# Kernel optimization log

Hardware: AMD Instinct MI355X
Metric: run time of the kernel (lower is better)

The kernel has to match this reference:

```python
import jax, jax.numpy as jnp
import numpy as np
from math import sqrt

THRESHOLD = 0.5
NEG_POS_RATIO = 3
ALPHA = 1.0


def make_priors():
    fms = [(38, 0.1, [1.0, 2.0, 0.5]), (19, 0.2, [1.0, 2.0, 0.5, 3.0, 1.0 / 3]),
           (10, 0.375, [1.0, 2.0, 0.5, 3.0, 1.0 / 3]), (5, 0.55, [1.0, 2.0, 0.5, 3.0, 1.0 / 3]),
           (3, 0.725, [1.0, 2.0, 0.5]), (1, 0.9, [1.0, 2.0, 0.5])]
    scales = [0.1, 0.2, 0.375, 0.55, 0.725, 0.9]
    priors = []
    for k, (d, s, ratios) in enumerate(fms):
        for i in range(d):
            for j in range(d):
                cx = (i + 0.5) / d
                cy = (j + 0.5) / d
                for r in ratios:
                    priors.append([cx, cy, s * sqrt(r), s / sqrt(r)])
                    if r == 1.0:
                        add = sqrt(scales[k] * scales[k + 1]) if k + 1 < len(scales) else 1.0
                        priors.append([cx, cy, add, add])
    return np.clip(np.asarray(priors, dtype=np.float32), 0.0, 1.0)  # [8732, 4]


def cxcy_to_xy(b):
    return jnp.concatenate([b[..., :2] - b[..., 2:] / 2.0, b[..., :2] + b[..., 2:] / 2.0], -1)


def jaccard(a, b):
    # a: [O,4] cxcy, b: [P,4] cxcy -> IoU [O,P]
    a_xy, b_xy = cxcy_to_xy(a), cxcy_to_xy(b)
    lt = jnp.maximum(a_xy[:, None, :2], b_xy[None, :, :2])
    rb = jnp.minimum(a_xy[:, None, 2:], b_xy[None, :, 2:])
    wh = jnp.clip(rb - lt, 0.0)
    inter = wh[..., 0] * wh[..., 1]
    area_a = (a_xy[:, 2] - a_xy[:, 0]) * (a_xy[:, 3] - a_xy[:, 1])
    area_b = (b_xy[:, 2] - b_xy[:, 0]) * (b_xy[:, 3] - b_xy[:, 1])
    return inter / (area_a[:, None] + area_b[None, :] - inter)


def cxcy_to_gcxgcy(cxcy, priors):
    g_cxcy = (cxcy[..., :2] - priors[..., :2]) / (priors[..., 2:] / 10.0)
    g_wh = jnp.log(cxcy[..., 2:] / priors[..., 2:]) * 5.0
    return jnp.concatenate([g_cxcy, g_wh], -1)


def match_one(boxes_i, priors):
    # boxes_i: [O,4] cxcy
    n_obj = boxes_i.shape[0]
    ov = jaccard(boxes_i, priors)                      # [O, P]
    ov_per_prior = ov.max(0)                           # [P]
    obj_per_prior = ov.argmax(0)                       # [P]
    prior_per_obj = ov.argmax(1)                       # [O]
    obj_per_prior = obj_per_prior.at[prior_per_obj].set(jnp.arange(n_obj))
    ov_per_prior = ov_per_prior.at[prior_per_obj].set(1.0)
    labels = (ov_per_prior >= THRESHOLD).astype(jnp.int32)  # [P], 1=text 0=bg
    true_locs = cxcy_to_gcxgcy(boxes_i[obj_per_prior], priors)  # [P,4]
    return labels, true_locs


def setup_inputs() -> dict:
    key = jax.random.key(0)
    k1, k2, k3, k4 = jax.random.split(key, 4)
    priors = jnp.asarray(make_priors())
    B, P, O = 512, priors.shape[0], 16
    predicted_locs = jax.random.normal(k1, (B, P, 4), dtype=jnp.float32)
    predicted_scores = jax.random.normal(k2, (B, P, 2), dtype=jnp.float32)
    centers = 0.2 + 0.6 * jax.random.uniform(k3, (B, O, 2), dtype=jnp.float32)
    wh = 0.05 + 0.35 * jax.random.uniform(k4, (B, O, 2), dtype=jnp.float32)
    boxes = jnp.concatenate([centers, wh], -1)  # cxcy format
    return {"predicted_locs": predicted_locs, "predicted_scores": predicted_scores,
            "boxes": boxes, "priors": priors}


def reference(predicted_locs, predicted_scores, boxes, priors):
    B, P, _ = predicted_locs.shape
    labels, true_locs = jax.vmap(match_one, in_axes=(0, None))(boxes, priors)  # [B,P], [B,P,4]
    pos = labels != 0
    mask = pos.astype(predicted_locs.dtype)            # [B,P]
    n_pos = pos.sum(1)                                 # [B]

    # localization L1 loss (mean over positive box coordinates)
    loc_abs = jnp.abs(predicted_locs - true_locs).sum(-1)  # [B,P]
    loc_loss = (loc_abs * mask).sum() / (mask.sum() * 4.0)

    # per-prior cross-entropy
    logp = jax.nn.log_softmax(predicted_scores, -1)
    ce = -jnp.take_along_axis(logp, labels[..., None], -1)[..., 0]  # [B,P]

    conf_pos = (ce * mask).sum()
    ce_neg = jnp.where(pos, 0.0, ce)
    ce_neg = jnp.sort(ce_neg, axis=1)[:, ::-1]         # descending
    hard = jnp.arange(P)[None, :] < (NEG_POS_RATIO * n_pos)[:, None]
    conf_hn = (ce_neg * hard.astype(ce_neg.dtype)).sum()
    conf_loss = (conf_pos + conf_hn) / n_pos.sum().astype(predicted_locs.dtype)
    return conf_loss + ALPHA * loc_loss
```

## Files before the change

kernel.cpp:

```cpp
#include <hip/hip_runtime.h>

#define NP 8732
#define NQ (NP / 4)
#define NPT 35
#define NO 16
#define BLK 256
#define NWAVE (BLK / 64)
#define SPLIT 4
#define CHUNK (NP / SPLIT)
#define NITER ((CHUNK + BLK - 1) / BLK)
#define BLKS 1024
#define NWAVES (BLKS / 64)
#define NPT2 9


__device__ __forceinline__ float rfl(float x) {
    return __uint_as_float(__builtin_amdgcn_readfirstlane(__float_as_uint(x)));
}

__global__ __launch_bounds__(BLK, 4) void match_kernel(
    const float* __restrict__ boxes,
    const float* __restrict__ priors,
    unsigned char* __restrict__ g_obj,
    float* __restrict__ g_bv,
    int*   __restrict__ g_bi)
{
    const int b    = blockIdx.x;
    const int s    = blockIdx.y;
    const int tid  = threadIdx.x;
    const int lane = tid & 63;
    const int wv   = tid >> 6;
    const int lo = s * CHUNK, hi = lo + CHUNK;

    __shared__ float s_pv[NWAVE][NO][16];
    __shared__ int   s_pi[NWAVE][NO][16];

    float sx0[NO], sy0[NO], sx1[NO], sy1[NO], ra[NO];
    {
        const float4* bx4 = (const float4*)(boxes + (size_t)b * NO * 4);
#pragma unroll
        for (int j = 0; j < NO; j++) {
            float4 o = bx4[j];
            float hx = o.z * 0.5f, hy = o.w * 0.5f;
            sx0[j] = rfl(o.x - hx); sy0[j] = rfl(o.y - hy);
            sx1[j] = rfl(o.x + hx); sy1[j] = rfl(o.y + hy);
            ra[j]  = o.z * o.w;
        }
    }

    float tbv[NO]; int tbp[NO];
#pragma unroll
    for (int j = 0; j < NO; j++) { tbv[j] = -1.0f; tbp[j] = lo; }

    unsigned char* obj_row = g_obj + (size_t)b * NP;
    for (int k = 0; k < NITER; k++) {
        int p0 = lo + tid + k * BLK;
        bool valid = p0 < hi;
        int p = valid ? p0 : hi - 1;
        float4 pr = ((const float4*)priors)[p];
        float px0 = pr.x - pr.z * 0.5f, py0 = pr.y - pr.w * 0.5f;
        float px1 = pr.x + pr.z * 0.5f, py1 = pr.y + pr.w * 0.5f;
        float areab = pr.z * pr.w;
        if (!valid) px0 = 4.0f;
        float bv = -1.0f; int bo = 0;
#pragma unroll
        for (int j = 0; j < NO; j++) {
            bool ov = (sx1[j] >= px0) && (px1 >= sx0[j]) &&
                      (sy1[j] >= py0) && (py1 >= sy0[j]);
            if (ov) {
                float ix0 = fmaxf(sx0[j], px0);
                float iy0 = fmaxf(sy0[j], py0);
                float ix1 = fminf(sx1[j], px1);
                float iy1 = fminf(sy1[j], py1);
                float iw = fmaxf(ix1 - ix0, 0.0f);
                float ih = fmaxf(iy1 - iy0, 0.0f);
                float inter = iw * ih;
                float den = ra[j] + areab - inter;
                float iou = inter * __builtin_amdgcn_rcpf(den);
                if (iou > bv)     { bv = iou; bo = j; }
                if (iou > tbv[j]) { tbv[j] = iou; tbp[j] = p; }
            }
        }
        if (valid) obj_row[p] = (unsigned char)(bo | ((bv >= 0.5f) ? 0x80 : 0));
    }

#pragma unroll
    for (int j = 0; j < NO; j++) {
        float v = tbv[j]; int i = tbp[j];
        float v2 = __shfl_down(v, 32, 64); int i2 = __shfl_down(i, 32, 64);
        if (v2 > v || (v2 == v && i2 < i)) { v = v2; i = i2; }
        v2 = __shfl_down(v, 16, 64); i2 = __shfl_down(i, 16, 64);
        if (v2 > v || (v2 == v && i2 < i)) { v = v2; i = i2; }
        if (lane < 16) { s_pv[wv][j][lane] = v; s_pi[wv][j][lane] = i; }
    }
    __syncthreads();
    {
        const int j = tid >> 4, e = tid & 15;
        float v = s_pv[0][j][e]; int i = s_pi[0][j][e];
#pragma unroll
        for (int w = 1; w < NWAVE; w++) {
            float v2 = s_pv[w][j][e]; int i2 = s_pi[w][j][e];
            if (v2 > v || (v2 == v && i2 < i)) { v = v2; i = i2; }
        }
#pragma unroll
        for (int off = 8; off >= 1; off >>= 1) {
            float v2 = __shfl_down(v, off, 16); int i2 = __shfl_down(i, off, 16);
            if (v2 > v || (v2 == v && i2 < i)) { v = v2; i = i2; }
        }
        if (e == 0) {
            g_bv[((size_t)b * NO + j) * SPLIT + s] = v;
            g_bi[((size_t)b * NO + j) * SPLIT + s] = i;
        }
    }
}

__device__ __forceinline__ int hist_select(unsigned* hist, unsigned* s_part,
                                           unsigned* s_csuf, unsigned* s_sel,
                                           unsigned& kk, int tid, int lane, int wv)
{
    if (tid < 256) {
        unsigned ps = 0;
#pragma unroll
        for (int i = 0; i < 16; i++) ps += hist[tid * 16 + i];
        s_part[tid] = ps;
    }
    __syncthreads();
    if (wv == 0) {
        unsigned c0 = s_part[4 * lane + 0], c1 = s_part[4 * lane + 1];
        unsigned c2 = s_part[4 * lane + 2], c3 = s_part[4 * lane + 3];
        unsigned g = c0 + c1 + c2 + c3;
        unsigned incl = g;
#pragma unroll
        for (int off = 1; off < 64; off <<= 1) {
            unsigned o = __shfl_down(incl, off, 64);
            if (lane + off < 64) incl += o;
        }
        unsigned excl = incl - g;
        s_csuf[4 * lane + 3] = excl;
        s_csuf[4 * lane + 2] = excl + c3;
        s_csuf[4 * lane + 1] = excl + c3 + c2;
        s_csuf[4 * lane + 0] = excl + c3 + c2 + c1;
    }
    __syncthreads();
    if (tid < 256) {
        unsigned base = s_csuf[tid];
        if (base < kk && kk <= base + s_part[tid]) {
            unsigned run = base;
            for (int i = 15; i >= 0; i--) {
                unsigned h = hist[tid * 16 + i];
                if (kk <= run + h) { s_sel[0] = (unsigned)(tid * 16 + i); s_sel[1] = kk - run; break; }
                run += h;
            }
        }
    }
    __syncthreads();
    kk = s_sel[1];
    return (int)s_sel[0];
}

__global__ __launch_bounds__(BLKS, 8) void loss2_kernel(
    const float* __restrict__ plocs,
    const float* __restrict__ pscores,
    const float* __restrict__ boxes,
    const float* __restrict__ priors,
    const unsigned char* __restrict__ g_obj,
    const float* __restrict__ g_bv,
    const int*   __restrict__ g_bi,
    float* __restrict__ loc_out,
    float* __restrict__ conf_out,
    int*   __restrict__ npos_out)
{
    const int b    = blockIdx.x;
    const int tid  = threadIdx.x;
    const int lane = tid & 63;
    const int wv   = tid >> 6;

    __shared__ unsigned char s_obj[NP];
    __shared__ unsigned s_hist[4096];
    __shared__ unsigned s_part[256];
    __shared__ unsigned s_csuf[256];
    __shared__ unsigned s_sel[2];
    __shared__ float s_bcw[NO][4];
    __shared__ int   s_bestp[NO];
    __shared__ float s_tval;
    __shared__ float s_fred[3 * NWAVES];
    __shared__ int   s_ired[NWAVES];

    const unsigned* objw = (const unsigned*)(g_obj + (size_t)b * NP);
    for (int i = tid; i < NP / 4; i += BLKS) ((unsigned*)s_obj)[i] = objw[i];
    if (tid < NO * 4) ((float*)s_bcw)[tid] = boxes[(size_t)b * NO * 4 + tid];
    if (tid < NO) {
        const float* bv = g_bv + ((size_t)b * NO + tid) * SPLIT;
        const int*   bi = g_bi + ((size_t)b * NO + tid) * SPLIT;
        float v = bv[0]; int i = bi[0];
#pragma unroll
        for (int s = 1; s < SPLIT; s++) {
            float v2 = bv[s]; int i2 = bi[s];
            if (v2 > v || (v2 == v && i2 < i)) { v = v2; i = i2; }
        }
        s_bestp[tid] = i;
    }
    __syncthreads();
    if (tid == 0) {
#pragma unroll
        for (int o = 0; o < NO; o++) s_obj[s_bestp[o]] = (unsigned char)(0x80 | o);
    }
    __syncthreads();

    float ce[NPT2];
    float loc_sum = 0.0f, conf_pos = 0.0f; int np = 0;
    const float2* sc2 = (const float2*)(pscores + (size_t)b * NP * 2);
    const float4* pl4 = (const float4*)(plocs  + (size_t)b * NP * 4);
#pragma unroll
    for (int k = 0; k < NPT2; k++) {
        int p = tid + k * BLKS;
        float v = 0.0f;
        if (p < NP) {
            unsigned m = s_obj[p];
            bool pos = (m & 0x80) != 0;
            float2 s = sc2[p];
            float mx = fmaxf(s.x, s.y);
            float dd = fabsf(s.x - s.y);
            float cev = mx + __logf(1.0f + __expf(-dd)) - (pos ? s.y : s.x);
            if (pos) {
                np++;
                conf_pos += cev;
                int o = m & 15;
                float4 pr = ((const float4*)priors)[p];
                float gx = (s_bcw[o][0] - pr.x) / (pr.z / 10.0f);
                float gy = (s_bcw[o][1] - pr.y) / (pr.w / 10.0f);
                float gw = __logf(s_bcw[o][2] / pr.z) * 5.0f;
                float gh = __logf(s_bcw[o][3] / pr.w) * 5.0f;
                float4 pl = pl4[p];
                loc_sum += fabsf(pl.x - gx) + fabsf(pl.y - gy)
                         + fabsf(pl.z - gw) + fabsf(pl.w - gh);
            } else {
                v = cev;
            }
        }
        ce[k] = v;
    }

    int npw = np;
    for (int off = 32; off; off >>= 1) npw += __shfl_down(npw, off, 64);
    if (lane == 0) s_ired[wv] = npw;
    __syncthreads();
    int n_pos = 0;
#pragma unroll
    for (int w = 0; w < NWAVES; w++) n_pos += s_ired[w];

    const int K = 3 * n_pos;
    const bool selAll = (K >= NP);
    float t = 0.0f;
    if (!selAll) {
        unsigned kk = (unsigned)K;
        for (int i = tid; i < 4096; i += BLKS) s_hist[i] = 0u;
        __syncthreads();
#pragma unroll
        for (int k = 0; k < NPT2; k++)
            atomicAdd(&s_hist[__float_as_uint(ce[k]) >> 19], 1u);
        __syncthreads();
        unsigned b1 = (unsigned)hist_select(s_hist, s_part, s_csuf, s_sel, kk, tid, lane, wv);
        unsigned cnt1 = s_hist[b1];
        if (cnt1 == 1u) {
#pragma unroll
            for (int k = 0; k < NPT2; k++)
                if ((__float_as_uint(ce[k]) >> 19) == b1) s_tval = ce[k];
            __syncthreads();
            t = s_tval;
        } else {
            __syncthreads();
            for (int i = tid; i < 4096; i += BLKS) s_hist[i] = 0u;
            __syncthreads();
#pragma unroll
            for (int k = 0; k < NPT2; k++) {
                unsigned u = __float_as_uint(ce[k]);
                if ((u >> 19) == b1) atomicAdd(&s_hist[(u >> 7) & 0xFFFu], 1u);
            }
            __syncthreads();
            unsigned b2 = (unsigned)hist_select(s_hist, s_part, s_csuf, s_sel, kk, tid, lane, wv);
            unsigned p2 = (b1 << 12) | b2;
            unsigned cnt2 = s_hist[b2];
            if (cnt2 == 1u) {
#pragma unroll
                for (int k = 0; k < NPT2; k++)
                    if ((__float_as_uint(ce[k]) >> 7) == p2) s_tval = ce[k];
                __syncthreads();
                t = s_tval;
            } else {
                __syncthreads();
                for (int i = tid; i < 4096; i += BLKS) s_hist[i] = 0u;
                __syncthreads();
#pragma unroll
                for (int k = 0; k < NPT2; k++) {
                    unsigned u = __float_as_uint(ce[k]);
                    if ((u >> 7) == p2) atomicAdd(&s_hist[u & 0x7Fu], 1u);
                }
                __syncthreads();
                unsigned b3 = (unsigned)hist_select(s_hist, s_part, s_csuf, s_sel, kk, tid, lane, wv);
                t = __uint_as_float((p2 << 7) | b3);
            }
        }
    }

    float sgt = 0.0f; int cgt = 0;
#pragma unroll
    for (int k = 0; k < NPT2; k++) {
        float v = ce[k];
        if (selAll || v > t) { sgt += v; cgt++; }
    }

    float a = sgt, c = conf_pos, l = loc_sum; int g = cgt;
    for (int off = 32; off; off >>= 1) {
        a += __shfl_down(a, off, 64);
        c += __shfl_down(c, off, 64);
        l += __shfl_down(l, off, 64);
        g += __shfl_down(g, off, 64);
    }
    __syncthreads();
    if (lane == 0) {
        s_fred[wv] = a; s_fred[NWAVES + wv] = c; s_fred[2 * NWAVES + wv] = l;
        s_ired[wv] = g;
    }
    __syncthreads();
    if (tid == 0) {
        float sa = 0.0f, sc = 0.0f, sl = 0.0f; int sg = 0;
#pragma unroll
        for (int w = 0; w < NWAVES; w++) {
            sa += s_fred[w]; sc += s_fred[NWAVES + w]; sl += s_fred[2 * NWAVES + w];
            sg += s_ired[w];
        }
        float conf_hn = selAll ? sa : (sa + (float)(K - sg) * t);
        conf_out[b] = sc + conf_hn;
        loc_out[b]  = sl;
        npos_out[b] = n_pos;
    }
}

__global__ __launch_bounds__(BLK, 2) void mbox_row_kernel(
    const float* __restrict__ plocs, const float* __restrict__ pscores,
    const float* __restrict__ boxes, const float* __restrict__ priors,
    float* __restrict__ loc_out, float* __restrict__ conf_out,
    int* __restrict__ npos_out)
{
    const int b = blockIdx.x, tid = threadIdx.x, lane = tid & 63, wv = tid >> 6;
    const int par = tid & 1, objLo = par << 3;
    __shared__ __align__(16) float s_ce[NP];
    __shared__ unsigned char s_obj[NP];
    __shared__ float s_bcw[NO][4], s_bxy[NO][4], s_barea[NO];
    __shared__ float s_redv[NO * NWAVE]; __shared__ int s_redi[NO * NWAVE];
    __shared__ int s_bestp[NO];
    __shared__ unsigned s_hist16[16];
    __shared__ float s_tval;
    __shared__ float s_fred[3 * NWAVE]; __shared__ int s_ired[NWAVE];

    if (tid < NO * 4) ((float*)s_bcw)[tid] = boxes[(size_t)b * NO * 4 + tid];
    __syncthreads();
    if (tid < NO) {
        float cx = s_bcw[tid][0], cy = s_bcw[tid][1], w = s_bcw[tid][2], h = s_bcw[tid][3];
        s_bxy[tid][0] = cx - w * 0.5f; s_bxy[tid][1] = cy - h * 0.5f;
        s_bxy[tid][2] = cx + w * 0.5f; s_bxy[tid][3] = cy + h * 0.5f;
        s_barea[tid] = w * h;
    }
    __syncthreads();
    float rx0[8], ry0[8], rx1[8], ry1[8], ra[8];
#pragma unroll
    for (int j = 0; j < 8; j++) {
        rx0[j] = s_bxy[objLo + j][0]; ry0[j] = s_bxy[objLo + j][1];
        rx1[j] = s_bxy[objLo + j][2]; ry1[j] = s_bxy[objLo + j][3];
        ra[j]  = s_barea[objLo + j];
    }
    float tbv[8]; int tbp[8];
#pragma unroll
    for (int j = 0; j < 8; j++) { tbv[j] = -1.0f; tbp[j] = 0; }
    for (int p = (tid >> 1); p < NP; p += (BLK / 2)) {
        float4 pr = ((const float4*)priors)[p];
        float px0 = pr.x - pr.z * 0.5f, py0 = pr.y - pr.w * 0.5f;
        float px1 = pr.x + pr.z * 0.5f, py1 = pr.y + pr.w * 0.5f;
        float areab = pr.z * pr.w;
        float bv = -1.0f; int bo = objLo;
#pragma unroll
        for (int j = 0; j < 8; j++) {
            float ix0 = fmaxf(rx0[j], px0), iy0 = fmaxf(ry0[j], py0);
            float ix1 = fminf(rx1[j], px1), iy1 = fminf(ry1[j], py1);
            float iw = fmaxf(ix1 - ix0, 0.0f), ih = fmaxf(iy1 - iy0, 0.0f);
            float inter = iw * ih, den = ra[j] + areab - inter;
            float iou = inter * __builtin_amdgcn_rcpf(den);
            if (iou > bv) { bv = iou; bo = objLo + j; }
            if (iou > tbv[j]) { tbv[j] = iou; tbp[j] = p; }
        }
        float vN = __shfl_xor(bv, 1, 64); int oN = __shfl_xor(bo, 1, 64);
        bool take = par ? (vN >= bv) : (vN > bv);
        if (take) { bv = vN; bo = oN; }
        if (par == 0) s_obj[p] = (unsigned char)(bo | ((bv >= 0.5f) ? 0x80 : 0));
    }
#pragma unroll
    for (int j = 0; j < 8; j++) {
        float v = tbv[j]; int i = tbp[j];
        for (int off = 32; off >= 2; off >>= 1) {
            float v2 = __shfl_down(v, off, 64); int i2 = __shfl_down(i, off, 64);
            if (v2 > v || (v2 == v && i2 < i)) { v = v2; i = i2; }
        }
        if (lane < 2) { s_redv[(objLo + j) * NWAVE + wv] = v; s_redi[(objLo + j) * NWAVE + wv] = i; }
    }
    __syncthreads();
    if (tid < NO) {
        float v = s_redv[tid * NWAVE]; int i = s_redi[tid * NWAVE];
#pragma unroll
        for (int w = 1; w < NWAVE; w++) {
            float v2 = s_redv[tid * NWAVE + w]; int i2 = s_redi[tid * NWAVE + w];
            if (v2 > v || (v2 == v && i2 < i)) { v = v2; i = i2; }
        }
        s_bestp[tid] = i;
    }
    __syncthreads();
    if (tid == 0) {
#pragma unroll
        for (int o = 0; o < NO; o++) s_obj[s_bestp[o]] = (unsigned char)(0x80 | o);
    }
    __syncthreads();
    float loc_sum = 0.0f, conf_pos = 0.0f; int np = 0;
    const float2* sc2 = (const float2*)(pscores + (size_t)b * NP * 2);
    const float4* pl4 = (const float4*)(plocs + (size_t)b * NP * 4);
    for (int p = tid; p < NP; p += BLK) {
        unsigned m = s_obj[p]; bool pos = (m & 0x80) != 0;
        float2 s = sc2[p];
        float mx = fmaxf(s.x, s.y), dd = fabsf(s.x - s.y);
        float cev = mx + __logf(1.0f + __expf(-dd)) - (pos ? s.y : s.x);
        if (pos) {
            np++; conf_pos += cev;
            int o = m & 15;
            float4 pr = ((const float4*)priors)[p];
            float gx = (s_bcw[o][0] - pr.x) / (pr.z / 10.0f);
            float gy = (s_bcw[o][1] - pr.y) / (pr.w / 10.0f);
            float gw = __logf(s_bcw[o][2] / pr.z) * 5.0f;
            float gh = __logf(s_bcw[o][3] / pr.w) * 5.0f;
            float4 pl = pl4[p];
            loc_sum += fabsf(pl.x - gx) + fabsf(pl.y - gy) + fabsf(pl.z - gw) + fabsf(pl.w - gh);
            s_ce[p] = 0.0f;
        } else s_ce[p] = cev;
    }
    int npw = np;
    for (int off = 32; off; off >>= 1) npw += __shfl_down(npw, off, 64);
    if (lane == 0) s_ired[wv] = npw;
    __syncthreads();
    int n_pos = 0;
#pragma unroll
    for (int w = 0; w < NWAVE; w++) n_pos += s_ired[w];
    const int K = 3 * n_pos; const bool selAll = (K >= NP);
    float t = 0.0f;
    const float4* ce4 = (const float4*)s_ce;
    if (!selAll) {
        unsigned prefix = 0u, kk = (unsigned)K; bool done = false;
        for (int shift = 28; shift >= 0 && !done; shift -= 4) {
            __syncthreads();
            if (tid < 16) s_hist16[tid] = 0u;
            __syncthreads();
            unsigned maskhi = (shift == 28) ? 0u : (0xFFFFFFFFu << (shift + 4));
            for (int q = tid; q < NQ; q += BLK) {
                float4 v = ce4[q];
#pragma unroll
                for (int j = 0; j < 4; j++) {
                    unsigned u = __float_as_uint(j == 0 ? v.x : j == 1 ? v.y : j == 2 ? v.z : v.w);
                    if ((u & maskhi) == prefix) atomicAdd(&s_hist16[(u >> shift) & 15u], 1u);
                }
            }
            __syncthreads();
            int dsel = 15; unsigned cnt;
            for (;; dsel--) { cnt = s_hist16[dsel]; if (kk <= cnt || dsel == 0) break; kk -= cnt; }
            prefix |= ((unsigned)dsel << shift);
            if (shift > 0 && cnt == 1u) {
                unsigned mh = 0xFFFFFFFFu << shift;
                for (int q = tid; q < NQ; q += BLK) {
                    float4 v = ce4[q];
#pragma unroll
                    for (int j = 0; j < 4; j++) {
                        float f = (j == 0 ? v.x : j == 1 ? v.y : j == 2 ? v.z : v.w);
                        if ((__float_as_uint(f) & mh) == prefix) s_tval = f;
                    }
                }
                __syncthreads();
                t = s_tval; done = true;
            } else if (shift == 0) t = __uint_as_float(prefix);
        }
    }
    float sgt = 0.0f; int cgt = 0;
    for (int q = tid; q < NQ; q += BLK) {
        float4 v = ce4[q];
        if (selAll || v.x > t) { sgt += v.x; cgt++; }
        if (selAll || v.y > t) { sgt += v.y; cgt++; }
        if (selAll || v.z > t) { sgt += v.z; cgt++; }
        if (selAll || v.w > t) { sgt += v.w; cgt++; }
    }
    float a = sgt, c = conf_pos, l = loc_sum; int g = cgt;
    for (int off = 32; off; off >>= 1) {
        a += __shfl_down(a, off, 64); c += __shfl_down(c, off, 64);
        l += __shfl_down(l, off, 64); g += __shfl_down(g, off, 64);
    }
    __syncthreads();
    if (lane == 0) { s_fred[wv] = a; s_fred[NWAVE + wv] = c; s_fred[2 * NWAVE + wv] = l; s_ired[wv] = g; }
    __syncthreads();
    if (tid == 0) {
        float sa = 0, sc = 0, sl = 0; int sg = 0;
#pragma unroll
        for (int w = 0; w < NWAVE; w++) { sa += s_fred[w]; sc += s_fred[NWAVE + w]; sl += s_fred[2 * NWAVE + w]; sg += s_ired[w]; }
        float conf_hn = selAll ? sa : (sa + (float)(K - sg) * t);
        conf_out[b] = sc + conf_hn; loc_out[b] = sl; npos_out[b] = n_pos;
    }
}

__global__ __launch_bounds__(256) void mbox_finalize_kernel(
    const float* __restrict__ loc_in, const float* __restrict__ conf_in,
    const int* __restrict__ npos_in, int B, float* __restrict__ out)
{
    __shared__ float sl[4], sc[4];
    __shared__ int si[4];
    int tid = threadIdx.x, lane = tid & 63, wv = tid >> 6;
    float l = 0.0f, c = 0.0f; int n = 0;
    for (int i = tid; i < B; i += 256) { l += loc_in[i]; c += conf_in[i]; n += npos_in[i]; }
    for (int off = 32; off; off >>= 1) {
        l += __shfl_down(l, off, 64);
        c += __shfl_down(c, off, 64);
        n += __shfl_down(n, off, 64);
    }
    if (lane == 0) { sl[wv] = l; sc[wv] = c; si[wv] = n; }
    __syncthreads();
    if (tid == 0) {
        float tl = sl[0] + sl[1] + sl[2] + sl[3];
        float tc = sc[0] + sc[1] + sc[2] + sc[3];
        int tn = si[0] + si[1] + si[2] + si[3];
        float fn = (float)tn;
        out[0] = tc / fn + tl / (fn * 4.0f);
    }
}

extern "C" void kernel_launch(void* const* d_in, const int* in_sizes, int n_in,
                              void* d_out, int out_size, void* d_ws, size_t ws_size,
                              hipStream_t stream) {
    const float* plocs   = (const float*)d_in[0];
    const float* pscores = (const float*)d_in[1];
    const float* boxes   = (const float*)d_in[2];
    const float* priors  = (const float*)d_in[3];
    const int B = in_sizes[0] / (NP * 4);

    float* loc_ws  = (float*)d_ws;
    float* conf_ws = loc_ws + B;
    int*   np_ws   = (int*)(conf_ws + B);
    float* g_bv    = (float*)(np_ws + B);
    int*   g_bi    = (int*)(g_bv + (size_t)B * NO * SPLIT);
    unsigned char* g_obj = (unsigned char*)(g_bi + (size_t)B * NO * SPLIT);
    size_t need = (size_t)(3 * B) * 4 + (size_t)B * NO * SPLIT * 8 + (size_t)B * NP;

    if (ws_size >= need) {
        match_kernel<<<dim3(B, SPLIT), BLK, 0, stream>>>(boxes, priors, g_obj, g_bv, g_bi);
        loss2_kernel<<<B, BLKS, 0, stream>>>(plocs, pscores, boxes, priors,
                                             g_obj, g_bv, g_bi,
                                             loc_ws, conf_ws, np_ws);
    } else {
        mbox_row_kernel<<<B, BLK, 0, stream>>>(plocs, pscores, boxes, priors,
                                               loc_ws, conf_ws, np_ws);
    }
    mbox_finalize_kernel<<<1, 256, 0, stream>>>(loc_ws, conf_ws, np_ws, B, (float*)d_out);
}
```

Measured before the change: 178.4 us.

## Fuse prior matching into loss kernel, keeping match results in shared memory

Measured after the change: 177.1 us. About the same (-0.7%).

```diff
diff --git a/kernel.cpp b/kernel.cpp
--- a/kernel.cpp
+++ b/kernel.cpp
@@ -1,14 +1,7 @@
 #include <hip/hip_runtime.h>
 
 #define NP 8732
-#define NQ (NP / 4)
-#define NPT 35
 #define NO 16
-#define BLK 256
-#define NWAVE (BLK / 64)
-#define SPLIT 4
-#define CHUNK (NP / SPLIT)
-#define NITER ((CHUNK + BLK - 1) / BLK)
 #define BLKS 1024
 #define NWAVES (BLKS / 64)
 #define NPT2 9
@@ -18,22 +11,78 @@
     return __uint_as_float(__builtin_amdgcn_readfirstlane(__float_as_uint(x)));
 }
 
-__global__ __launch_bounds__(BLK, 4) void match_kernel(
+__device__ __forceinline__ int hist_select(unsigned* hist, unsigned* s_part,
+                                           unsigned* s_csuf, unsigned* s_sel,
+                                           unsigned& kk, int tid, int lane, int wv)
+{
+    if (tid < 256) {
+        unsigned ps = 0;
+#pragma unroll
+        for (int i = 0; i < 16; i++) ps += hist[tid * 16 + i];
+        s_part[tid] = ps;
+    }
+    __syncthreads();
+    if (wv == 0) {
+        unsigned c0 = s_part[4 * lane + 0], c1 = s_part[4 * lane + 1];
+        unsigned c2 = s_part[4 * lane + 2], c3 = s_part[4 * lane + 3];
+        unsigned g = c0 + c1 + c2 + c3;
+        unsigned incl = g;
+#pragma unroll
+        for (int off = 1; off < 64; off <<= 1) {
+            unsigned o = __shfl_down(incl, off, 64);
+            if (lane + off < 64) incl += o;
+        }
+        unsigned excl = incl - g;
+        s_csuf[4 * lane + 3] = excl;
+        s_csuf[4 * lane + 2] = excl + c3;
+        s_csuf[4 * lane + 1] = excl + c3 + c2;
+        s_csuf[4 * lane + 0] = excl + c3 + c2 + c1;
+    }
+    __syncthreads();
+    if (tid < 256) {
+        unsigned base = s_csuf[tid];
+        if (base < kk && kk <= base + s_part[tid]) {
+            unsigned run = base;
+            for (int i = 15; i >= 0; i--) {
+                unsigned h = hist[tid * 16 + i];
+                if (kk <= run + h) { s_sel[0] = (unsigned)(tid * 16 + i); s_sel[1] = kk - run; break; }
+                run += h;
+            }
+        }
+    }
+    __syncthreads();
+    kk = s_sel[1];
+    return (int)s_sel[0];
+}
+
+__global__ __launch_bounds__(BLKS, 8) void fused_kernel(
+    const float* __restrict__ plocs,
+    const float* __restrict__ pscores,
     const float* __restrict__ boxes,
     const float* __restrict__ priors,
-    unsigned char* __restrict__ g_obj,
-    float* __restrict__ g_bv,
-    int*   __restrict__ g_bi)
+    float* __restrict__ loc_out,
+    float* __restrict__ conf_out,
+    int*   __restrict__ npos_out)
 {
     const int b    = blockIdx.x;
-    const int s    = blockIdx.y;
     const int tid  = threadIdx.x;
     const int lane = tid & 63;
     const int wv   = tid >> 6;
-    const int lo = s * CHUNK, hi = lo + CHUNK;
-
-    __shared__ float s_pv[NWAVE][NO][16];
-    __shared__ int   s_pi[NWAVE][NO][16];
+
+    __shared__ unsigned char s_obj[NP];
+    __shared__ unsigned s_hist[4096];
+    __shared__ float s_pv[NWAVES][NO][16];
+    __shared__ int   s_pi[NWAVES][NO][16];
+    __shared__ unsigned s_part[256];
+    __shared__ unsigned s_csuf[256];
+    __shared__ unsigned s_sel[2];
+    __shared__ float s_bcw[NO][4];
+    __shared__ int   s_bestp[NO];
+    __shared__ float s_tval;
+    __shared__ float s_fred[3 * NWAVES];
+    __shared__ int   s_ired[NWAVES];
+
+    if (tid < NO * 4) ((float*)s_bcw)[tid] = boxes[(size_t)b * NO * 4 + tid];
 
     float sx0[NO], sy0[NO], sx1[NO], sy1[NO], ra[NO];
     {
@@ -50,13 +99,12 @@
 
     float tbv[NO]; int tbp[NO];
 #pragma unroll
-    for (int j = 0; j < NO; j++) { tbv[j] = -1.0f; tbp[j] = lo; }
-
-    unsigned char* obj_row = g_obj + (size_t)b * NP;
-    for (int k = 0; k < NITER; k++) {
-        int p0 = lo + tid + k * BLK;
-        bool valid = p0 < hi;
-        int p = valid ? p0 : hi - 1;
+    for (int j = 0; j < NO; j++) { tbv[j] = -1.0f; tbp[j] = 0; }
+
+    for (int k = 0; k < NPT2; k++) {
+        int p0 = tid + k * BLKS;
+        bool valid = p0 < NP;
+        int p = valid ? p0 : NP - 1;
         float4 pr = ((const float4*)priors)[p];
         float px0 = pr.x - pr.z * 0.5f, py0 = pr.y - pr.w * 0.5f;
         float px1 = pr.x + pr.z * 0.5f, py1 = pr.y + pr.w * 0.5f;
@@ -81,7 +129,7 @@
                 if (iou > tbv[j]) { tbv[j] = iou; tbp[j] = p; }
             }
         }
-        if (valid) obj_row[p] = (unsigned char)(bo | ((bv >= 0.5f) ? 0x80 : 0));
+        if (valid) s_obj[p] = (unsigned char)(bo | ((bv >= 0.5f) ? 0x80 : 0));
     }
 
 #pragma unroll
@@ -94,11 +142,11 @@
         if (lane < 16) { s_pv[wv][j][lane] = v; s_pi[wv][j][lane] = i; }
     }
     __syncthreads();
-    {
+    if (tid < 256) {
         const int j = tid >> 4, e = tid & 15;
         float v = s_pv[0][j][e]; int i = s_pi[0][j][e];
 #pragma unroll
-        for (int w = 1; w < NWAVE; w++) {
+        for (int w = 1; w < NWAVES; w++) {
             float v2 = s_pv[w][j][e]; int i2 = s_pi[w][j][e];
             if (v2 > v || (v2 == v && i2 < i)) { v = v2; i = i2; }
         }
@@ -107,98 +155,7 @@
             float v2 = __shfl_down(v, off, 16); int i2 = __shfl_down(i, off, 16);
             if (v2 > v || (v2 == v && i2 < i)) { v = v2; i = i2; }
         }
-        if (e == 0) {
-            g_bv[((size_t)b * NO + j) * SPLIT + s] = v;
-            g_bi[((size_t)b * NO + j) * SPLIT + s] = i;
-        }
-    }
-}
-
-__device__ __forceinline__ int hist_select(unsigned* hist, unsigned* s_part,
-                                           unsigned* s_csuf, unsigned* s_sel,
-                                           unsigned& kk, int tid, int lane, int wv)
-{
-    if (tid < 256) {
-        unsigned ps = 0;
-#pragma unroll
-        for (int i = 0; i < 16; i++) ps += hist[tid * 16 + i];
-        s_part[tid] = ps;
-    }
-    __syncthreads();
-    if (wv == 0) {
-        unsigned c0 = s_part[4 * lane + 0], c1 = s_part[4 * lane + 1];
-        unsigned c2 = s_part[4 * lane + 2], c3 = s_part[4 * lane + 3];
-        unsigned g = c0 + c1 + c2 + c3;
-        unsigned incl = g;
-#pragma unroll
-        for (int off = 1; off < 64; off <<= 1) {
-            unsigned o = __shfl_down(incl, off, 64);
-            if (lane + off < 64) incl += o;
-        }
-        unsigned excl = incl - g;
-        s_csuf[4 * lane + 3] = excl;
-        s_csuf[4 * lane + 2] = excl + c3;
-        s_csuf[4 * lane + 1] = excl + c3 + c2;
-        s_csuf[4 * lane + 0] = excl + c3 + c2 + c1;
-    }
-    __syncthreads();
-    if (tid < 256) {
-        unsigned base = s_csuf[tid];
-        if (base < kk && kk <= base + s_part[tid]) {
-            unsigned run = base;
-            for (int i = 15; i >= 0; i--) {
-                unsigned h = hist[tid * 16 + i];
-                if (kk <= run + h) { s_sel[0] = (unsigned)(tid * 16 + i); s_sel[1] = kk - run; break; }
-                run += h;
-            }
-        }
-    }
-    __syncthreads();
-    kk = s_sel[1];
-    return (int)s_sel[0];
-}
-
-__global__ __launch_bounds__(BLKS, 8) void loss2_kernel(
-    const float* __restrict__ plocs,
-    const float* __restrict__ pscores,
-    const float* __restrict__ boxes,
-    const float* __restrict__ priors,
-    const unsigned char* __restrict__ g_obj,
-    const float* __restrict__ g_bv,
-    const int*   __restrict__ g_bi,
-    float* __restrict__ loc_out,
-    float* __restrict__ conf_out,
-    int*   __restrict__ npos_out)
-{
-    const int b    = blockIdx.x;
-    const int tid  = threadIdx.x;
-    const int lane = tid & 63;
-    const int wv   = tid >> 6;
-
-    __shared__ unsigned char s_obj[NP];
-    __shared__ unsigned s_hist[4096];
-    __shared__ unsigned s_part[256];
-    __shared__ unsigned s_csuf[256];
-    __shared__ unsigned s_sel[2];
-    __shared__ float s_bcw[NO][4];
-    __shared__ int   s_bestp[NO];
-    __shared__ float s_tval;
-    __shared__ float s_fred[3 * NWAVES];
-    __shared__ int   s_ired[NWAVES];
-
-    const unsigned* objw = (const unsigned*)(g_obj + (size_t)b * NP);
-    for (int i = tid; i < NP / 4; i += BLKS) ((unsigned*)s_obj)[i] = objw[i];
-    if (tid < NO * 4) ((float*)s_bcw)[tid] = boxes[(size_t)b * NO * 4 + tid];
-    if (tid < NO) {
-        const float* bv = g_bv + ((size_t)b * NO + tid) * SPLIT;
-        const int*   bi = g_bi + ((size_t)b * NO + tid) * SPLIT;
-        float v = bv[0]; int i = bi[0];
-#pragma unroll
-        for (int s = 1; s < SPLIT; s++) {
-            float v2 = bv[s]; int i2 = bi[s];
-            if (v2 > v || (v2 == v && i2 < i)) { v = v2; i = i2; }
-        }
-        s_bestp[tid] = i;
+        if (e == 0) s_bestp[j] = i;
     }
     __syncthreads();
     if (tid == 0) {
@@ -337,178 +294,6 @@
     }
 }
 
-__global__ __launch_bounds__(BLK, 2) void mbox_row_kernel(
-    const float* __restrict__ plocs, const float* __restrict__ pscores,
-    const float* __restrict__ boxes, const float* __restrict__ priors,
-    float* __restrict__ loc_out, float* __restrict__ conf_out,
-    int* __restrict__ npos_out)
-{
-    const int b = blockIdx.x, tid = threadIdx.x, lane = tid & 63, wv = tid >> 6;
-    const int par = tid & 1, objLo = par << 3;
-    __shared__ __align__(16) float s_ce[NP];
-    __shared__ unsigned char s_obj[NP];
-    __shared__ float s_bcw[NO][4], s_bxy[NO][4], s_barea[NO];
-    __shared__ float s_redv[NO * NWAVE]; __shared__ int s_redi[NO * NWAVE];
-    __shared__ int s_bestp[NO];
-    __shared__ unsigned s_hist16[16];
-    __shared__ float s_tval;
-    __shared__ float s_fred[3 * NWAVE]; __shared__ int s_ired[NWAVE];
-
-    if (tid < NO * 4) ((float*)s_bcw)[tid] = boxes[(size_t)b * NO * 4 + tid];
-    __syncthreads();
-    if (tid < NO) {
-        float cx = s_bcw[tid][0], cy = s_bcw[tid][1], w = s_bcw[tid][2], h = s_bcw[tid][3];
-        s_bxy[tid][0] = cx - w * 0.5f; s_bxy[tid][1] = cy - h * 0.5f;
-        s_bxy[tid][2] = cx + w * 0.5f; s_bxy[tid][3] = cy + h * 0.5f;
-        s_barea[tid] = w * h;
-    }
-    __syncthreads();
-    float rx0[8], ry0[8], rx1[8], ry1[8], ra[8];
-#pragma unroll
-    for (int j = 0; j < 8; j++) {
-        rx0[j] = s_bxy[objLo + j][0]; ry0[j] = s_bxy[objLo + j][1];
-        rx1[j] = s_bxy[objLo + j][2]; ry1[j] = s_bxy[objLo + j][3];
-        ra[j]  = s_barea[objLo + j];
-    }
-    float tbv[8]; int tbp[8];
-#pragma unroll
-    for (int j = 0; j < 8; j++) { tbv[j] = -1.0f; tbp[j] = 0; }
-    for (int p = (tid >> 1); p < NP; p += (BLK / 2)) {
-        float4 pr = ((const float4*)priors)[p];
-        float px0 = pr.x - pr.z * 0.5f, py0 = pr.y - pr.w * 0.5f;
-        float px1 = pr.x + pr.z * 0.5f, py1 = pr.y + pr.w * 0.5f;
-        float areab = pr.z * pr.w;
-        float bv = -1.0f; int bo = objLo;
-#pragma unroll
-        for (int j = 0; j < 8; j++) {
-            float ix0 = fmaxf(rx0[j], px0), iy0 = fmaxf(ry0[j], py0);
-            float ix1 = fminf(rx1[j], px1), iy1 = fminf(ry1[j], py1);
-            float iw = fmaxf(ix1 - ix0, 0.0f), ih = fmaxf(iy1 - iy0, 0.0f);
-            float inter = iw * ih, den = ra[j] + areab - inter;
-            float iou = inter * __builtin_amdgcn_rcpf(den);
-            if (iou > bv) { bv = iou; bo = objLo + j; }
-            if (iou > tbv[j]) { tbv[j] = iou; tbp[j] = p; }
-        }
-        float vN = __shfl_xor(bv, 1, 64); int oN = __shfl_xor(bo, 1, 64);
-        bool take = par ? (vN >= bv) : (vN > bv);
-        if (take) { bv = vN; bo = oN; }
-        if (par == 0) s_obj[p] = (unsigned char)(bo | ((bv >= 0.5f) ? 0x80 : 0));
-    }
-#pragma unroll
-    for (int j = 0; j < 8; j++) {
-        float v = tbv[j]; int i = tbp[j];
-        for (int off = 32; off >= 2; off >>= 1) {
-            float v2 = __shfl_down(v, off, 64); int i2 = __shfl_down(i, off, 64);
-            if (v2 > v || (v2 == v && i2 < i)) { v = v2; i = i2; }
-        }
-        if (lane < 2) { s_redv[(objLo + j) * NWAVE + wv] = v; s_redi[(objLo + j) * NWAVE + wv] = i; }
-    }
-    __syncthreads();
-    if (tid < NO) {
-        float v = s_redv[tid * NWAVE]; int i = s_redi[tid * NWAVE];
-#pragma unroll
-        for (int w = 1; w < NWAVE; w++) {
-            float v2 = s_redv[tid * NWAVE + w]; int i2 = s_redi[tid * NWAVE + w];
-            if (v2 > v || (v2 == v && i2 < i)) { v = v2; i = i2; }
-        }
-        s_bestp[tid] = i;
-    }
-    __syncthreads();
-    if (tid == 0) {
-#pragma unroll
-        for (int o = 0; o < NO; o++) s_obj[s_bestp[o]] = (unsigned char)(0x80 | o);
-    }
-    __syncthreads();
-    float loc_sum = 0.0f, conf_pos = 0.0f; int np = 0;
-    const float2* sc2 = (const float2*)(pscores + (size_t)b * NP * 2);
-    const float4* pl4 = (const float4*)(plocs + (size_t)b * NP * 4);
-    for (int p = tid; p < NP; p += BLK) {
-        unsigned m = s_obj[p]; bool pos = (m & 0x80) != 0;
-        float2 s = sc2[p];
-        float mx = fmaxf(s.x, s.y), dd = fabsf(s.x - s.y);
-        float cev = mx + __logf(1.0f + __expf(-dd)) - (pos ? s.y : s.x);
-        if (pos) {
-            np++; conf_pos += cev;
-            int o = m & 15;
-            float4 pr = ((const float4*)priors)[p];
-            float gx = (s_bcw[o][0] - pr.x) / (pr.z / 10.0f);
-            float gy = (s_bcw[o][1] - pr.y) / (pr.w / 10.0f);
-            float gw = __logf(s_bcw[o][2] / pr.z) * 5.0f;
-            float gh = __logf(s_bcw[o][3] / pr.w) * 5.0f;
-            float4 pl = pl4[p];
-            loc_sum += fabsf(pl.x - gx) + fabsf(pl.y - gy) + fabsf(pl.z - gw) + fabsf(pl.w - gh);
-            s_ce[p] = 0.0f;
-        } else s_ce[p] = cev;
-    }
-    int npw = np;
-    for (int off = 32; off; off >>= 1) npw += __shfl_down(npw, off, 64);
-    if (lane == 0) s_ired[wv] = npw;
-    __syncthreads();
-    int n_pos = 0;
-#pragma unroll
-    for (int w = 0; w < NWAVE; w++) n_pos += s_ired[w];
-    const int K = 3 * n_pos; const bool selAll = (K >= NP);
-    float t = 0.0f;
-    const float4* ce4 = (const float4*)s_ce;
-    if (!selAll) {
-        unsigned prefix = 0u, kk = (unsigned)K; bool done = false;
-        for (int shift = 28; shift >= 0 && !done; shift -= 4) {
-            __syncthreads();
-            if (tid < 16) s_hist16[tid] = 0u;
-            __syncthreads();
-            unsigned maskhi = (shift == 28) ? 0u : (0xFFFFFFFFu << (shift + 4));
-            for (int q = tid; q < NQ; q += BLK) {
-                float4 v = ce4[q];
-#pragma unroll
-                for (int j = 0; j < 4; j++) {
-                    unsigned u = __float_as_uint(j == 0 ? v.x : j == 1 ? v.y : j == 2 ? v.z : v.w);
-                    if ((u & maskhi) == prefix) atomicAdd(&s_hist16[(u >> shift) & 15u], 1u);
-                }
-            }
-            __syncthreads();
-            int dsel = 15; unsigned cnt;
-            for (;; dsel--) { cnt = s_hist16[dsel]; if (kk <= cnt || dsel == 0) break; kk -= cnt; }
-            prefix |= ((unsigned)dsel << shift);
-            if (shift > 0 && cnt == 1u) {
-                unsigned mh = 0xFFFFFFFFu << shift;
-                for (int q = tid; q < NQ; q += BLK) {
-                    float4 v = ce4[q];
-#pragma unroll
-                    for (int j = 0; j < 4; j++) {
-                        float f = (j == 0 ? v.x : j == 1 ? v.y : j == 2 ? v.z : v.w);
-                        if ((__float_as_uint(f) & mh) == prefix) s_tval = f;
-                    }
-                }
-                __syncthreads();
-                t = s_tval; done = true;
-            } else if (shift == 0) t = __uint_as_float(prefix);
-        }
-    }
-    float sgt = 0.0f; int cgt = 0;
-    for (int q = tid; q < NQ; q += BLK) {
-        float4 v = ce4[q];
-        if (selAll || v.x > t) { sgt += v.x; cgt++; }
-        if (selAll || v.y > t) { sgt += v.y; cgt++; }
-        if (selAll || v.z > t) { sgt += v.z; cgt++; }
-        if (selAll || v.w > t) { sgt += v.w; cgt++; }
-    }
-    float a = sgt, c = conf_pos, l = loc_sum; int g = cgt;
-    for (int off = 32; off; off >>= 1) {
-        a += __shfl_down(a, off, 64); c += __shfl_down(c, off, 64);
-        l += __shfl_down(l, off, 64); g += __shfl_down(g, off, 64);
-    }
-    __syncthreads();
-    if (lane == 0) { s_fred[wv] = a; s_fred[NWAVE + wv] = c; s_fred[2 * NWAVE + wv] = l; s_ired[wv] = g; }
-    __syncthreads();
-    if (tid == 0) {
-        float sa = 0, sc = 0, sl = 0; int sg = 0;
-#pragma unroll
-        for (int w = 0; w < NWAVE; w++) { sa += s_fred[w]; sc += s_fred[NWAVE + w]; sl += s_fred[2 * NWAVE + w]; sg += s_ired[w]; }
-        float conf_hn = selAll ? sa : (sa + (float)(K - sg) * t);
-        conf_out[b] = sc + conf_hn; loc_out[b] = sl; npos_out[b] = n_pos;
-    }
-}
-
 __global__ __launch_bounds__(256) void mbox_finalize_kernel(
     const float* __restrict__ loc_in, const float* __restrict__ conf_in,
     const int* __restrict__ npos_in, int B, float* __restrict__ out)
@@ -546,19 +331,8 @@
     float* loc_ws  = (float*)d_ws;
     float* conf_ws = loc_ws + B;
     int*   np_ws   = (int*)(conf_ws + B);
-    float* g_bv    = (float*)(np_ws + B);
-    int*   g_bi    = (int*)(g_bv + (size_t)B * NO * SPLIT);
-    unsigned char* g_obj = (unsigned char*)(g_bi + (size_t)B * NO * SPLIT);
-    size_t need = (size_t)(3 * B) * 4 + (size_t)B * NO * SPLIT * 8 + (size_t)B * NP;
-
-    if (ws_size >= need) {
-        match_kernel<<<dim3(B, SPLIT), BLK, 0, stream>>>(boxes, priors, g_obj, g_bv, g_bi);
-        loss2_kernel<<<B, BLKS, 0, stream>>>(plocs, pscores, boxes, priors,
-                                             g_obj, g_bv, g_bi,
-                                             loc_ws, conf_ws, np_ws);
-    } else {
-        mbox_row_kernel<<<B, BLK, 0, stream>>>(plocs, pscores, boxes, priors,
-                                               loc_ws, conf_ws, np_ws);
-    }
+
+    fused_kernel<<<B, BLKS, 0, stream>>>(plocs, pscores, boxes, priors,
+                                         loc_ws, conf_ws, np_ws);
     mbox_finalize_kernel<<<1, 256, 0, stream>>>(loc_ws, conf_ws, np_ws, B, (float*)d_out);
 }
```
